# Kernel tuning notes

Hardware: AMD Instinct MI355X
Metric: run time of the kernel (lower is better)

Reference implementation:

```python
import jax, jax.numpy as jnp
import numpy as np

TEMP = 0.08
EPS = 1e-8
GAMMA = 0.99
BETA = 0.5 * (1.0 - GAMMA)  # alpha * (1 - gamma)
COS_EPS = 1e-8  # torch F.cosine_similarity norm-product clamp


def setup_inputs() -> dict:
    key = jax.random.key(0)
    k1, k2, k3 = jax.random.split(key, 3)
    B, D, C = 8192, 256, 7
    features = jax.random.normal(k1, (B, D), dtype=jnp.float32)
    labels = jax.random.randint(k2, (B,), 0, C)
    # orthogonal prototypes via QR, as in generate_orthogonal_vectors
    q, _ = jnp.linalg.qr(jax.random.normal(k3, (D, C), dtype=jnp.float32))
    prototypes = q.T  # [C, D]
    momentums = jnp.zeros((C, D), dtype=jnp.float32)
    return {"features": features, "labels": labels,
            "prototypes": prototypes, "momentums": momentums}


def _update_prototypes(features, labels, prototypes, momentums):
    # sequential EMA over the batch (repeated labels chain), as in the torch loop
    deltas = features - prototypes[labels]  # delta uses the OLD prototypes throughout

    def step(m, ld):
        l, d = ld
        return m.at[l].set(GAMMA * m[l] + BETA * d), None

    m_final, _ = jax.lax.scan(step, momentums, (labels, deltas))
    target = prototypes + m_final  # [C, D]
    q, _ = jnp.linalg.qr(target.T)  # reduced QR: [D, C]
    return q.T  # [C, D], re-orthogonalized prototypes


def reference(features, labels, prototypes, momentums):
    C = prototypes.shape[0]
    new_protos = _update_prototypes(features, labels, prototypes, momentums)

    feats = jnp.concatenate([features, new_protos], axis=0)          # [N, D]
    labs = jnp.concatenate([labels, jnp.arange(C, dtype=labels.dtype)])
    N = feats.shape[0]

    # cosine similarity matrix: dot / clamp(|x||y|, eps)  (matches F.cosine_similarity)
    nrm = jnp.linalg.norm(feats, axis=-1)                            # [N]
    sim = (feats @ feats.T) / jnp.maximum(nrm[:, None] * nrm[None, :], COS_EPS)
    scores = (1.0 + sim) * 0.5 + EPS

    offdiag = 1.0 - jnp.eye(N, dtype=scores.dtype)
    scores = scores * offdiag / TEMP
    scores = scores - jnp.max(scores)

    same = labs[:, None] == labs[None, :]                            # [N, N] bool
    pos_mask = same.astype(scores.dtype) * offdiag
    neg_mask = (~same).astype(scores.dtype)

    pos = jnp.sum(scores * pos_mask, axis=-1) / (jnp.sum(pos_mask, axis=-1) + EPS)
    neg = jnp.log(jnp.sum(jnp.exp(scores) * neg_mask, axis=-1) + EPS)
    loss = -pos + neg                                                # [N]

    m = loss > 0
    cnt = jnp.sum(m.astype(loss.dtype))
    mean_pos = jnp.sum(jnp.where(m, loss, 0.0)) / jnp.maximum(cnt, 1.0)
    return jnp.where(cnt > 0, mean_pos, jnp.array(0.0, loss.dtype))
```

## Files before the change

### kernel.cpp

```cpp
#include <hip/hip_runtime.h>
#include <stdint.h>

#define B    8192
#define D    256
#define C    7
#define NTOT 8199
#define NPAD 8320
#define NT   65
#define NBLK 2145
#define BETAC 0.005f
#define L2GAMMA (-0.0144995696951151f)

using f32x4  = __attribute__((ext_vector_type(4))) float;

__device__ __forceinline__ void async16(const void* src, void* dst) {
    __builtin_amdgcn_global_load_lds(
        (const __attribute__((address_space(1))) void*)src,
        (__attribute__((address_space(3))) void*)dst, 16, 0, 0);
}

__device__ __forceinline__ float score_of(float sim) {
    return fmaf(sim, 6.25f, 6.25f + 1.25e-7f);
}

#define WAITVM(N) asm volatile("s_waitcnt vmcnt(" #N ")" ::: "memory")
#define BARRIER() do { __builtin_amdgcn_s_barrier(); asm volatile("" ::: "memory"); } while(0)

__global__ void kprep(const int* __restrict__ labels, float* __restrict__ wbuf,
                      int* __restrict__ labs_ext, int* __restrict__ hist,
                      float* __restrict__ S, float* __restrict__ lossacc,
                      unsigned* __restrict__ ticket) {
    __shared__ int cnt[256 * 8];
    __shared__ int tot[8];
    int t = threadIdx.x;
    int lane = t & 63, w = t >> 6;
    for (int i = t; i < C * 256; i += 256) S[i] = 0.f;
    if (t == 0) { lossacc[0] = 0.f; lossacc[1] = 0.f; *ticket = 0u; }
    int lab[32];
    #pragma unroll
    for (int q = 0; q < 8; ++q) {
        int4 v = *(const int4*)(labels + t * 32 + q * 4);
        lab[q * 4 + 0] = v.x; lab[q * 4 + 1] = v.y;
        lab[q * 4 + 2] = v.z; lab[q * 4 + 3] = v.w;
    }
    int myc[8] = {0, 0, 0, 0, 0, 0, 0, 0};
    #pragma unroll
    for (int k = 0; k < 32; ++k) {
        #pragma unroll
        for (int cc = 0; cc < 7; ++cc) myc[cc] += (lab[k] == cc) ? 1 : 0;
    }
    #pragma unroll
    for (int cc = 0; cc < 8; ++cc) cnt[t * 8 + cc] = myc[cc];
    __syncthreads();
    for (int c = w; c < C; c += 4) {
        int v[4], partial = 0;
        #pragma unroll
        for (int k = 0; k < 4; ++k) { v[k] = cnt[(lane * 4 + k) * 8 + c]; partial += v[k]; }
        int inc = partial;
        #pragma unroll
        for (int d = 1; d < 64; d <<= 1) {
            int y = __shfl_up(inc, d);
            if (lane >= d) inc += y;
        }
        int run = inc - partial;
        #pragma unroll
        for (int k = 0; k < 4; ++k) { int tmp = v[k]; cnt[(lane * 4 + k) * 8 + c] = run; run += tmp; }
        if (lane == 63) { tot[c] = inc; hist[c] = inc; }
    }
    __syncthreads();
    #pragma unroll 4
    for (int k = 0; k < 32; ++k) {
        int idx = t * 32 + k;
        int c = lab[k];
        int r = ++cnt[t * 8 + c];
        int kk = tot[c] - r;
        wbuf[idx] = exp2f((float)kk * L2GAMMA);
    }
    for (int i = t; i < NPAD; i += 256)
        labs_ext[i] = (i < B) ? labels[i] : ((i < NTOT) ? (i - B) : -1);
}

__global__ void kaccnorm(const float* __restrict__ feats, const int* __restrict__ labels,
                         const float* __restrict__ wbuf, float* __restrict__ S,
                         unsigned* __restrict__ G32) {
    __shared__ float sacc[4][7][256];
    int tid = threadIdx.x, lane = tid & 63, wv = tid >> 6;
    float acc7[7][4] = {};
    int base = blockIdx.x * 32 + wv * 8;
    for (int k = 0; k < 8; ++k) {
        int row = base + k;
        const float4 v = *(const float4*)(feats + (size_t)row * 256 + lane * 4);
        float ss = v.x * v.x + v.y * v.y + v.z * v.z + v.w * v.w;
        #pragma unroll
        for (int off = 1; off < 64; off <<= 1) ss += __shfl_xor(ss, off);
        float rn = 1.f / sqrtf(ss);
        unsigned p = (unsigned)__builtin_amdgcn_cvt_pk_fp8_f32(v.x * rn, v.y * rn, 0, false);
        p = (unsigned)__builtin_amdgcn_cvt_pk_fp8_f32(v.z * rn, v.w * rn, (int)p, true);
        G32[(size_t)row * 64 + lane] = p;
        int c = labels[row];
        float wgt = wbuf[row];
        float w0 = v.x * wgt, w1 = v.y * wgt, w2 = v.z * wgt, w3 = v.w * wgt;
        #pragma unroll
        for (int cc = 0; cc < 7; ++cc)
            if (c == cc) { acc7[cc][0] += w0; acc7[cc][1] += w1; acc7[cc][2] += w2; acc7[cc][3] += w3; }
    }
    #pragma unroll
    for (int cc = 0; cc < 7; ++cc) {
        #pragma unroll
        for (int jj = 0; jj < 4; ++jj)
            sacc[wv][cc][lane * 4 + jj] = acc7[cc][jj];
    }
    __syncthreads();
    #pragma unroll
    for (int cc = 0; cc < 7; ++cc) {
        float s = sacc[0][cc][tid] + sacc[1][cc][tid] + sacc[2][cc][tid] + sacc[3][cc][tid];
        atomicAdd(&S[cc * 256 + tid], s);
    }
    if (blockIdx.x < NPAD - NTOT && tid < 64)
        G32[(size_t)(NTOT + blockIdx.x) * 64 + tid] = 0u;
}

__global__ void kproto(const float* __restrict__ S, const int* __restrict__ hist,
                       const float* __restrict__ protos, const float* __restrict__ moms,
                       unsigned char* __restrict__ G8) {
    __shared__ float A[256 * 8];
    __shared__ float V[256 * 8];
    __shared__ float vvs[8];
    __shared__ float bcast[8];
    int t = threadIdx.x;
    int lane = t & 63, w = t >> 6;
    #pragma unroll
    for (int c = 0; c < C; ++c) {
        float p = protos[c * 256 + t];
        float m0 = moms[c * 256 + t];
        float gn = exp2f((float)hist[c] * L2GAMMA);
        float mf = gn * m0 + BETAC * S[c * 256 + t] - 0.5f * (1.f - gn) * p;
        A[t * 8 + c] = p + mf;
        V[t * 8 + c] = 0.f;
    }
    __syncthreads();
    for (int j = 0; j < C; ++j) {
        if (w == 0) {
            float s = 0.f;
            for (int i = lane; i < 256; i += 64) {
                float a = (i >= j) ? A[i * 8 + j] : 0.f;
                s += a * a;
            }
            #pragma unroll
            for (int off = 32; off; off >>= 1) s += __shfl_xor(s, off);
            if (lane == 0) {
                float norm = sqrtf(s);
                float alpha = A[j * 8 + j];
                float beta = (alpha >= 0.f) ? -norm : norm;
                float vv = 2.f * beta * (beta - alpha);
                bcast[0] = alpha; bcast[1] = beta;
                bcast[2] = (vv > 0.f) ? 1.f : 0.f;
                vvs[j] = (vv > 0.f) ? vv : 1.f;
            }
        }
        __syncthreads();
        float alpha = bcast[0], valid = bcast[2];
        float beta = bcast[1];
        float vi = 0.f;
        if (valid != 0.f) {
            if (t == j) vi = alpha - beta;
            else if (t > j) vi = A[t * 8 + j];
        }
        V[t * 8 + j] = vi;
        __syncthreads();
        float vvj = vvs[j];
        for (int k = j + 1 + w; k < C; k += 4) {
            float cp = 0.f;
            for (int i = lane; i < 256; i += 64) cp += V[i * 8 + j] * A[i * 8 + k];
            #pragma unroll
            for (int off = 32; off; off >>= 1) cp += __shfl_xor(cp, off);
            float scale = 2.f * cp / vvj;
            for (int i = lane; i < 256; i += 64) A[i * 8 + k] -= scale * V[i * 8 + j];
        }
        __syncthreads();
    }
    #pragma unroll
    for (int c = 0; c < C; ++c) A[t * 8 + c] = (t == c) ? 1.f : 0.f;
    __syncthreads();
    for (int j = C - 1; j >= 0; --j) {
        float vvj = vvs[j];
        for (int k = w; k < C; k += 4) {
            float cp = 0.f;
            for (int i = lane; i < 256; i += 64) cp += V[i * 8 + j] * A[i * 8 + k];
            #pragma unroll
            for (int off = 32; off; off >>= 1) cp += __shfl_xor(cp, off);
            float scale = 2.f * cp / vvj;
            for (int i = lane; i < 256; i += 64) A[i * 8 + k] -= scale * V[i * 8 + j];
        }
        __syncthreads();
    }
    for (int c = w; c < C; c += 4) {
        float s = 0.f;
        for (int i = lane; i < 256; i += 64) { float a = A[i * 8 + c]; s += a * a; }
        #pragma unroll
        for (int off = 32; off; off >>= 1) s += __shfl_xor(s, off);
        if (lane == 0) bcast[c] = 1.f / sqrtf(s);
    }
    __syncthreads();
    #pragma unroll
    for (int c = 0; c < C; ++c) {
        int pk = __builtin_amdgcn_cvt_pk_fp8_f32(A[t * 8 + c] * bcast[c], 0.f, 0, false);
        G8[(size_t)(B + c) * 256 + t] = (unsigned char)(pk & 0xff);
    }
}

__global__ __launch_bounds__(512, 2) void kmain(const unsigned char* __restrict__ G,
                                                const int* __restrict__ labs,
                                                float* __restrict__ pP,
                                                float* __restrict__ pN) {
    __shared__ unsigned char Asm_[128 * 256];
    __shared__ unsigned char Bsm_[128 * 256];
    float* rowP = (float*)Asm_;
    float* rowN = rowP + 256;
    float* colP = rowN + 256;
    float* colN = colP + 512;

    int b0 = blockIdx.x;
    int xcd = b0 & 7, pos = b0 >> 3;
    int b = (xcd == 0) ? pos : (269 + (xcd - 1) * 268 + pos);

    int jt = (int)((sqrtf(8.f * (float)b + 1.f) - 1.f) * 0.5f);
    while ((jt * (jt + 1)) / 2 > b) --jt;
    while (((jt + 1) * (jt + 2)) / 2 <= b) ++jt;
    int it = b - (jt * (jt + 1)) / 2;

    int rowA = it * 128, rowB = jt * 128;
    int tid = threadIdx.x, lane = tid & 63, w8 = tid >> 6;
    int wr = w8 >> 1, wc = w8 & 1;
    int g4 = lane >> 4, q15 = lane & 15;

    const char* gb = (const char*)G;

    #pragma unroll
    for (int q = 0; q < 4; ++q) {
        int o = q * 8192 + tid * 16;
        int row = o >> 8, colb = o & 255;
        int sc = colb ^ ((row & 15) << 4);
        async16(gb + (size_t)(rowA + row) * 256 + sc, (char*)Asm_ + o);
    }
    #pragma unroll
    for (int q = 0; q < 4; ++q) {
        int o = q * 8192 + tid * 16;
        int row = o >> 8, colb = o & 255;
        int sc = colb ^ ((row & 15) << 4);
        async16(gb + (size_t)(rowB + row) * 256 + sc, (char*)Bsm_ + o);
    }

    int ljv[4];
    #pragma unroll
    for (int n = 0; n < 4; ++n) ljv[n] = labs[rowB + wc * 64 + n * 16 + q15];
    int4 lrow[2];
    #pragma unroll
    for (int m = 0; m < 2; ++m)
        lrow[m] = *(const int4*)(labs + rowA + wr * 32 + m * 16 + g4 * 4);

    f32x4 acc[2][4];
    #pragma unroll
    for (int m = 0; m < 2; ++m)
        #pragma unroll
        for (int n = 0; n < 4; ++n) acc[m][n] = 0.f;

    WAITVM(0);
    BARRIER();

    #pragma unroll
    for (int kk = 0; kk < 8; ++kk) {
        long af[2], bfr[4];
        int cb = (kk * 32 + g4 * 8) ^ (q15 << 4);
        #pragma unroll
        for (int m = 0; m < 2; ++m) {
            int r0 = wr * 32 + m * 16 + q15;
            af[m] = *(const long*)((const char*)Asm_ + r0 * 256 + cb);
        }
        #pragma unroll
        for (int n = 0; n < 4; ++n) {
            int r0 = wc * 64 + n * 16 + q15;
            bfr[n] = *(const long*)((const char*)Bsm_ + r0 * 256 + cb);
        }
        __builtin_amdgcn_s_setprio(1);
        #pragma unroll
        for (int m = 0; m < 2; ++m)
            #pragma unroll
            for (int n = 0; n < 4; ++n)
                acc[m][n] = __builtin_amdgcn_mfma_f32_16x16x32_fp8_fp8(af[m], bfr[n], acc[m][n], 0, 0, 0);
        __builtin_amdgcn_s_setprio(0);
    }

    __syncthreads();

    float cs[4] = {0.f, 0.f, 0.f, 0.f}, cn[4] = {0.f, 0.f, 0.f, 0.f};
    bool fastpath = (it != jt) && (jt != NT - 1);

#define EPI(VALIDEXPR)                                                         \
    _Pragma("unroll")                                                          \
    for (int m = 0; m < 2; ++m) {                                              \
        _Pragma("unroll")                                                      \
        for (int r = 0; r < 4; ++r) {                                          \
            int il = wr * 32 + m * 16 + g4 * 4 + r;                            \
            int i = rowA + il; (void)i;                                        \
            int li = ((const int*)&lrow[m])[r];                                \
            float ps = 0.f, ns = 0.f;                                          \
            _Pragma("unroll")                                                  \
            for (int n = 0; n < 4; ++n) {                                      \
                int j = rowB + wc * 64 + n * 16 + q15; (void)j;                \
                float sim = acc[m][n][r];                                      \
                float s = score_of(sim);                                       \
                float e = __expf(s);                                           \
                if (VALIDEXPR) {                                               \
                    if (li == ljv[n]) { ps += s; cs[n] += s; }                 \
                    else              { ns += e; cn[n] += e; }                 \
                }                                                              \
            }                                                                  \
            _Pragma("unroll")                                                  \
            for (int off = 1; off < 16; off <<= 1) {                           \
                ps += __shfl_xor(ps, off);                                     \
                ns += __shfl_xor(ns, off);                                     \
            }                                                                  \
            if (q15 == 0) { rowP[wc * 128 + il] = ps; rowN[wc * 128 + il] = ns; } \
        }                                                                      \
    }

    if (fastpath) { EPI(true); }
    else          { EPI(i < NTOT && j < NTOT && i != j); }
#undef EPI

    #pragma unroll
    for (int n = 0; n < 4; ++n) {
        float a = cs[n], bb = cn[n];
        a += __shfl_xor(a, 16); a += __shfl_xor(a, 32);
        bb += __shfl_xor(bb, 16); bb += __shfl_xor(bb, 32);
        if (g4 == 0) {
            colP[wr * 128 + wc * 64 + n * 16 + q15] = a;
            colN[wr * 128 + wc * 64 + n * 16 + q15] = bb;
        }
    }

    __syncthreads();
    if (tid < 128) {
        pP[(size_t)jt * NPAD + rowA + tid] = rowP[tid] + rowP[128 + tid];
        pN[(size_t)jt * NPAD + rowA + tid] = rowN[tid] + rowN[128 + tid];
    } else if (tid < 256 && it != jt) {
        int tt = tid - 128;
        pP[(size_t)it * NPAD + rowB + tt] = colP[tt] + colP[128 + tt] + colP[256 + tt] + colP[384 + tt];
        pN[(size_t)it * NPAD + rowB + tt] = colN[tt] + colN[128 + tt] + colN[256 + tt] + colN[384 + tt];
    }
}

__global__ void kreduce(const float* __restrict__ pP, const float* __restrict__ pN,
                        const int* __restrict__ hist, const int* __restrict__ labs,
                        float* __restrict__ lossacc, unsigned* __restrict__ ticket,
                        float* __restrict__ out) {
    int i = blockIdx.x * 256 + threadIdx.x;
    float lsum = 0.f, lcnt = 0.f;
    if (i < NTOT) {
        float sp = 0.f, sn = 0.f;
        #pragma unroll 5
        for (int c = 0; c < NT; ++c) {
            sp += pP[(size_t)c * NPAD + i];
            sn += pN[(size_t)c * NPAD + i];
        }
        float cnt = (float)hist[labs[i]];
        float pos = sp / (cnt + 1e-8f);
        float neg = logf(sn + 1e-8f);
        float loss = neg - pos;
        if (loss > 0.f) { lsum = loss; lcnt = 1.f; }
    }
    #pragma unroll
    for (int off = 1; off < 64; off <<= 1) {
        lsum += __shfl_xor(lsum, off);
        lcnt += __shfl_xor(lcnt, off);
    }
    __shared__ float s1[4], s2[4];
    int lane = threadIdx.x & 63, w = threadIdx.x >> 6;
    if (lane == 0) { s1[w] = lsum; s2[w] = lcnt; }
    __syncthreads();
    if (threadIdx.x == 0) {
        atomicAdd(&lossacc[0], s1[0] + s1[1] + s1[2] + s1[3]);
        atomicAdd(&lossacc[1], s2[0] + s2[1] + s2[2] + s2[3]);
        __threadfence();
        unsigned tk = atomicAdd(ticket, 1u);
        if (tk == 32) {
            float a = atomicAdd(&lossacc[0], 0.f);
            float c2 = atomicAdd(&lossacc[1], 0.f);
            out[0] = (c2 > 0.f) ? a / fmaxf(c2, 1.f) : 0.f;
        }
    }
}

extern "C" void kernel_launch(void* const* d_in, const int* in_sizes, int n_in,
                              void* d_out, int out_size, void* d_ws, size_t ws_size,
                              hipStream_t stream) {
    const float* feats  = (const float*)d_in[0];
    const int*   labels = (const int*)d_in[1];
    const float* protos = (const float*)d_in[2];
    const float* moms   = (const float*)d_in[3];
    float* out = (float*)d_out;

    char* ws = (char*)d_ws;
    float*    S_      = (float*)(ws + 0);
    int*      hist    = (int*)  (ws + 7168);
    float*    lossacc = (float*)(ws + 7200);
    unsigned* ticket  = (unsigned*)(ws + 7208);
    float*    wbuf    = (float*)(ws + 7296);
    int*      labs    = (int*)  (ws + 40064);
    unsigned char* G  = (unsigned char*)(ws + 73344);
    float*    pP      = (float*)(ws + 2203264);
    float*    pN      = (float*)(ws + 4366464);

    kprep<<<1, 256, 0, stream>>>(labels, wbuf, labs, hist, S_, lossacc, ticket);
    kaccnorm<<<256, 256, 0, stream>>>(feats, labels, wbuf, S_, (unsigned*)G);
    kproto<<<1, 256, 0, stream>>>(S_, hist, protos, moms, G);
    kmain<<<NBLK, 512, 0, stream>>>(G, labs, pP, pN);
    kreduce<<<33, 256, 0, stream>>>(pP, pN, hist, labs, lossacc, ticket, out);
}
```

Before: 105.0 us.

## Compute positive sums via per-class sums of normalized features instead of in GEMM

The positive term is computed algebraically: each row's sum of same-label similarities equals its dot product with the class sum of normalized features, so the main tile epilogue accumulates only masked exp for negatives. Per-class normalized-feature sums are built alongside the EMA accumulation, and the final reduce does a 256-wide dot per row. The single-block prep kernel is merged into the accumulation kernel, which now writes per-block partials instead of using atomics. The exp uses exp2 with folded constants. This risks precision differences, since the positive sum now comes from fp32 features rather than the fp8 similarities used in the GEMM.

```diff
diff --git a/kernel.cpp b/kernel.cpp
--- a/kernel.cpp
+++ b/kernel.cpp
@@ -10,6 +10,10 @@
 #define NBLK 2145
 #define BETAC 0.005f
 #define L2GAMMA (-0.0144995696951151f)
+#define KC   (6.25f + 1.25e-7f)
+#define EC1  9.016844005555771f
+#define EC0  9.016844185925551f
+#define KACCB 128
 
 using f32x4  = __attribute__((ext_vector_type(4))) float;
 
@@ -19,23 +23,21 @@
         (__attribute__((address_space(3))) void*)dst, 16, 0, 0);
 }
 
-__device__ __forceinline__ float score_of(float sim) {
-    return fmaf(sim, 6.25f, 6.25f + 1.25e-7f);
-}
-
 #define WAITVM(N) asm volatile("s_waitcnt vmcnt(" #N ")" ::: "memory")
 #define BARRIER() do { __builtin_amdgcn_s_barrier(); asm volatile("" ::: "memory"); } while(0)
 
-__global__ void kprep(const int* __restrict__ labels, float* __restrict__ wbuf,
-                      int* __restrict__ labs_ext, int* __restrict__ hist,
-                      float* __restrict__ S, float* __restrict__ lossacc,
-                      unsigned* __restrict__ ticket) {
+__global__ void kaccnorm(const float* __restrict__ feats, const int* __restrict__ labels,
+                         float* __restrict__ Spart, float* __restrict__ CSpart,
+                         unsigned* __restrict__ G32, int* __restrict__ labs_ext,
+                         int* __restrict__ hist, float* __restrict__ lossacc,
+                         unsigned* __restrict__ ticket) {
     __shared__ int cnt[256 * 8];
     __shared__ int tot[8];
-    int t = threadIdx.x;
-    int lane = t & 63, w = t >> 6;
-    for (int i = t; i < C * 256; i += 256) S[i] = 0.f;
-    if (t == 0) { lossacc[0] = 0.f; lossacc[1] = 0.f; *ticket = 0u; }
+    __shared__ float wrow[64];
+    __shared__ float sacc[4][7][256];
+    int t = threadIdx.x, lane = t & 63, w = t >> 6;
+    int bid = blockIdx.x;
+
     int lab[32];
     #pragma unroll
     for (int q = 0; q < 8; ++q) {
@@ -65,76 +67,98 @@
         int run = inc - partial;
         #pragma unroll
         for (int k = 0; k < 4; ++k) { int tmp = v[k]; cnt[(lane * 4 + k) * 8 + c] = run; run += tmp; }
-        if (lane == 63) { tot[c] = inc; hist[c] = inc; }
-    }
-    __syncthreads();
-    #pragma unroll 4
-    for (int k = 0; k < 32; ++k) {
-        int idx = t * 32 + k;
-        int c = lab[k];
-        int r = ++cnt[t * 8 + c];
-        int kk = tot[c] - r;
-        wbuf[idx] = exp2f((float)kk * L2GAMMA);
-    }
-    for (int i = t; i < NPAD; i += 256)
-        labs_ext[i] = (i < B) ? labels[i] : ((i < NTOT) ? (i - B) : -1);
-}
-
-__global__ void kaccnorm(const float* __restrict__ feats, const int* __restrict__ labels,
-                         const float* __restrict__ wbuf, float* __restrict__ S,
-                         unsigned* __restrict__ G32) {
-    __shared__ float sacc[4][7][256];
-    int tid = threadIdx.x, lane = tid & 63, wv = tid >> 6;
+        if (lane == 63) { tot[c] = inc; if (bid == 0) hist[c] = inc; }
+    }
+    __syncthreads();
+    if (t < 2) {
+        int ch = 2 * bid + t;
+        int loc[7];
+        #pragma unroll
+        for (int cc = 0; cc < 7; ++cc) loc[cc] = cnt[ch * 8 + cc];
+        for (int k = 0; k < 32; ++k) {
+            int c2 = labels[ch * 32 + k];
+            int r = ++loc[c2];
+            wrow[t * 32 + k] = exp2f((float)(tot[c2] - r) * L2GAMMA);
+        }
+    }
+    if (t < 64) labs_ext[bid * 64 + t] = labels[bid * 64 + t];
+    if (bid == 0) {
+        if (t == 0) { lossacc[0] = 0.f; lossacc[1] = 0.f; *ticket = 0u; }
+        if (t < 128) { int i2 = B + t; labs_ext[i2] = (i2 < NTOT) ? (i2 - B) : -1; }
+        for (int idx = t; idx < 121 * 64; idx += 256) G32[NTOT * 64 + idx] = 0u;
+    }
+    __syncthreads();
+
     float acc7[7][4] = {};
-    int base = blockIdx.x * 32 + wv * 8;
-    for (int k = 0; k < 8; ++k) {
+    float cs7[7][4] = {};
+    int base = bid * 64 + w * 16;
+    for (int k = 0; k < 16; ++k) {
         int row = base + k;
         const float4 v = *(const float4*)(feats + (size_t)row * 256 + lane * 4);
         float ss = v.x * v.x + v.y * v.y + v.z * v.z + v.w * v.w;
         #pragma unroll
         for (int off = 1; off < 64; off <<= 1) ss += __shfl_xor(ss, off);
         float rn = 1.f / sqrtf(ss);
-        unsigned p = (unsigned)__builtin_amdgcn_cvt_pk_fp8_f32(v.x * rn, v.y * rn, 0, false);
-        p = (unsigned)__builtin_amdgcn_cvt_pk_fp8_f32(v.z * rn, v.w * rn, (int)p, true);
+        float g0 = v.x * rn, g1 = v.y * rn, g2 = v.z * rn, g3 = v.w * rn;
+        unsigned p = (unsigned)__builtin_amdgcn_cvt_pk_fp8_f32(g0, g1, 0, false);
+        p = (unsigned)__builtin_amdgcn_cvt_pk_fp8_f32(g2, g3, (int)p, true);
         G32[(size_t)row * 64 + lane] = p;
         int c = labels[row];
-        float wgt = wbuf[row];
-        float w0 = v.x * wgt, w1 = v.y * wgt, w2 = v.z * wgt, w3 = v.w * wgt;
+        float wgt = wrow[w * 16 + k];
         #pragma unroll
         for (int cc = 0; cc < 7; ++cc)
-            if (c == cc) { acc7[cc][0] += w0; acc7[cc][1] += w1; acc7[cc][2] += w2; acc7[cc][3] += w3; }
-    }
-    #pragma unroll
-    for (int cc = 0; cc < 7; ++cc) {
-        #pragma unroll
-        for (int jj = 0; jj < 4; ++jj)
-            sacc[wv][cc][lane * 4 + jj] = acc7[cc][jj];
-    }
-    __syncthreads();
-    #pragma unroll
-    for (int cc = 0; cc < 7; ++cc) {
-        float s = sacc[0][cc][tid] + sacc[1][cc][tid] + sacc[2][cc][tid] + sacc[3][cc][tid];
-        atomicAdd(&S[cc * 256 + tid], s);
-    }
-    if (blockIdx.x < NPAD - NTOT && tid < 64)
-        G32[(size_t)(NTOT + blockIdx.x) * 64 + tid] = 0u;
-}
-
-__global__ void kproto(const float* __restrict__ S, const int* __restrict__ hist,
-                       const float* __restrict__ protos, const float* __restrict__ moms,
-                       unsigned char* __restrict__ G8) {
+            if (c == cc) {
+                acc7[cc][0] += wgt * v.x; acc7[cc][1] += wgt * v.y;
+                acc7[cc][2] += wgt * v.z; acc7[cc][3] += wgt * v.w;
+                cs7[cc][0] += g0; cs7[cc][1] += g1;
+                cs7[cc][2] += g2; cs7[cc][3] += g3;
+            }
+    }
+    #pragma unroll
+    for (int cc = 0; cc < 7; ++cc)
+        #pragma unroll
+        for (int jj = 0; jj < 4; ++jj) sacc[w][cc][lane * 4 + jj] = acc7[cc][jj];
+    __syncthreads();
+    #pragma unroll
+    for (int cc = 0; cc < 7; ++cc)
+        Spart[(size_t)bid * 1792 + cc * 256 + t] =
+            sacc[0][cc][t] + sacc[1][cc][t] + sacc[2][cc][t] + sacc[3][cc][t];
+    __syncthreads();
+    #pragma unroll
+    for (int cc = 0; cc < 7; ++cc)
+        #pragma unroll
+        for (int jj = 0; jj < 4; ++jj) sacc[w][cc][lane * 4 + jj] = cs7[cc][jj];
+    __syncthreads();
+    #pragma unroll
+    for (int cc = 0; cc < 7; ++cc)
+        CSpart[(size_t)bid * 1792 + cc * 256 + t] =
+            sacc[0][cc][t] + sacc[1][cc][t] + sacc[2][cc][t] + sacc[3][cc][t];
+}
+
+__global__ void kproto(const float* __restrict__ Spart, const float* __restrict__ CSpart,
+                       const int* __restrict__ hist, const float* __restrict__ protos,
+                       const float* __restrict__ moms, unsigned char* __restrict__ G8,
+                       float* __restrict__ CSfin, float* __restrict__ Pnorm) {
     __shared__ float A[256 * 8];
     __shared__ float V[256 * 8];
     __shared__ float vvs[8];
     __shared__ float bcast[8];
     int t = threadIdx.x;
     int lane = t & 63, w = t >> 6;
+    float ssum[7] = {}, cssum[7] = {};
+    for (int b2 = 0; b2 < KACCB; ++b2) {
+        #pragma unroll
+        for (int cc = 0; cc < 7; ++cc) {
+            ssum[cc]  += Spart[(size_t)b2 * 1792 + cc * 256 + t];
+            cssum[cc] += CSpart[(size_t)b2 * 1792 + cc * 256 + t];
+        }
+    }
     #pragma unroll
     for (int c = 0; c < C; ++c) {
         float p = protos[c * 256 + t];
         float m0 = moms[c * 256 + t];
         float gn = exp2f((float)hist[c] * L2GAMMA);
-        float mf = gn * m0 + BETAC * S[c * 256 + t] - 0.5f * (1.f - gn) * p;
+        float mf = gn * m0 + BETAC * ssum[c] - 0.5f * (1.f - gn) * p;
         A[t * 8 + c] = p + mf;
         V[t * 8 + c] = 0.f;
     }
@@ -204,21 +228,21 @@
     __syncthreads();
     #pragma unroll
     for (int c = 0; c < C; ++c) {
-        int pk = __builtin_amdgcn_cvt_pk_fp8_f32(A[t * 8 + c] * bcast[c], 0.f, 0, false);
+        float val = A[t * 8 + c] * bcast[c];
+        int pk = __builtin_amdgcn_cvt_pk_fp8_f32(val, 0.f, 0, false);
         G8[(size_t)(B + c) * 256 + t] = (unsigned char)(pk & 0xff);
+        Pnorm[c * 256 + t] = val;
+        CSfin[c * 256 + t] = cssum[c] + val;
     }
 }
 
 __global__ __launch_bounds__(512, 2) void kmain(const unsigned char* __restrict__ G,
                                                 const int* __restrict__ labs,
-                                                float* __restrict__ pP,
                                                 float* __restrict__ pN) {
     __shared__ unsigned char Asm_[128 * 256];
     __shared__ unsigned char Bsm_[128 * 256];
-    float* rowP = (float*)Asm_;
-    float* rowN = rowP + 256;
-    float* colP = rowN + 256;
-    float* colN = colP + 512;
+    float* rowN = (float*)Asm_;
+    float* colN = rowN + 256;
 
     int b0 = blockIdx.x;
     int xcd = b0 & 7, pos = b0 >> 3;
@@ -293,7 +317,7 @@
 
     __syncthreads();
 
-    float cs[4] = {0.f, 0.f, 0.f, 0.f}, cn[4] = {0.f, 0.f, 0.f, 0.f};
+    float cn[4] = {0.f, 0.f, 0.f, 0.f};
     bool fastpath = (it != jt) && (jt != NT - 1);
 
 #define EPI(VALIDEXPR)                                                         \
@@ -304,24 +328,19 @@
             int il = wr * 32 + m * 16 + g4 * 4 + r;                            \
             int i = rowA + il; (void)i;                                        \
             int li = ((const int*)&lrow[m])[r];                                \
-            float ps = 0.f, ns = 0.f;                                          \
+            float ns = 0.f;                                                    \
             _Pragma("unroll")                                                  \
             for (int n = 0; n < 4; ++n) {                                      \
                 int j = rowB + wc * 64 + n * 16 + q15; (void)j;                \
                 float sim = acc[m][n][r];                                      \
-                float s = score_of(sim);                                       \
-                float e = __expf(s);                                           \
-                if (VALIDEXPR) {                                               \
-                    if (li == ljv[n]) { ps += s; cs[n] += s; }                 \
-                    else              { ns += e; cn[n] += e; }                 \
-                }                                                              \
+                float e = exp2f(fmaf(sim, EC1, EC0));                          \
+                bool keep = (VALIDEXPR) && (li != ljv[n]);                     \
+                float me = keep ? e : 0.f;                                     \
+                ns += me; cn[n] += me;                                         \
             }                                                                  \
             _Pragma("unroll")                                                  \
-            for (int off = 1; off < 16; off <<= 1) {                           \
-                ps += __shfl_xor(ps, off);                                     \
-                ns += __shfl_xor(ns, off);                                     \
-            }                                                                  \
-            if (q15 == 0) { rowP[wc * 128 + il] = ps; rowN[wc * 128 + il] = ns; } \
+            for (int off = 1; off < 16; off <<= 1) ns += __shfl_xor(ns, off);  \
+            if (q15 == 0) rowN[wc * 128 + il] = ns;                            \
         }                                                                      \
     }
 
@@ -331,41 +350,61 @@
 
     #pragma unroll
     for (int n = 0; n < 4; ++n) {
-        float a = cs[n], bb = cn[n];
+        float a = cn[n];
         a += __shfl_xor(a, 16); a += __shfl_xor(a, 32);
-        bb += __shfl_xor(bb, 16); bb += __shfl_xor(bb, 32);
-        if (g4 == 0) {
-            colP[wr * 128 + wc * 64 + n * 16 + q15] = a;
-            colN[wr * 128 + wc * 64 + n * 16 + q15] = bb;
-        }
+        if (g4 == 0) colN[wr * 128 + wc * 64 + n * 16 + q15] = a;
     }
 
     __syncthreads();
     if (tid < 128) {
-        pP[(size_t)jt * NPAD + rowA + tid] = rowP[tid] + rowP[128 + tid];
         pN[(size_t)jt * NPAD + rowA + tid] = rowN[tid] + rowN[128 + tid];
     } else if (tid < 256 && it != jt) {
         int tt = tid - 128;
-        pP[(size_t)it * NPAD + rowB + tt] = colP[tt] + colP[128 + tt] + colP[256 + tt] + colP[384 + tt];
         pN[(size_t)it * NPAD + rowB + tt] = colN[tt] + colN[128 + tt] + colN[256 + tt] + colN[384 + tt];
     }
 }
 
-__global__ void kreduce(const float* __restrict__ pP, const float* __restrict__ pN,
+__global__ void kreduce(const float* __restrict__ pN, const float* __restrict__ feats,
+                        const float* __restrict__ Pnorm, const float* __restrict__ CSfin,
                         const int* __restrict__ hist, const int* __restrict__ labs,
                         float* __restrict__ lossacc, unsigned* __restrict__ ticket,
                         float* __restrict__ out) {
-    int i = blockIdx.x * 256 + threadIdx.x;
+    __shared__ float cls[7 * 264];
+    int tid = threadIdx.x;
+    for (int idx = tid; idx < 7 * 256; idx += 256)
+        cls[(idx >> 8) * 264 + (idx & 255)] = CSfin[idx];
+    __syncthreads();
+
+    int i = blockIdx.x * 256 + tid;
     float lsum = 0.f, lcnt = 0.f;
     if (i < NTOT) {
-        float sp = 0.f, sn = 0.f;
+        float sn = 0.f;
         #pragma unroll 5
-        for (int c = 0; c < NT; ++c) {
-            sp += pP[(size_t)c * NPAD + i];
-            sn += pN[(size_t)c * NPAD + i];
-        }
-        float cnt = (float)hist[labs[i]];
-        float pos = sp / (cnt + 1e-8f);
+        for (int c = 0; c < NT; ++c) sn += pN[(size_t)c * NPAD + i];
+
+        int c = labs[i];
+        const float* cv = cls + c * 264;
+        float dot = 0.f;
+        if (i < B) {
+            float ss = 0.f;
+            const float* fr = feats + (size_t)i * 256;
+            for (int k4 = 0; k4 < 64; ++k4) {
+                float4 v = *(const float4*)(fr + k4 * 4);
+                float4 cvv = *(const float4*)(cv + k4 * 4);
+                ss += v.x * v.x + v.y * v.y + v.z * v.z + v.w * v.w;
+                dot += v.x * cvv.x + v.y * cvv.y + v.z * cvv.z + v.w * cvv.w;
+            }
+            dot *= 1.f / sqrtf(ss);
+        } else {
+            const float* pr = Pnorm + (size_t)(i - B) * 256;
+            for (int k4 = 0; k4 < 64; ++k4) {
+                float4 v = *(const float4*)(pr + k4 * 4);
+                float4 cvv = *(const float4*)(cv + k4 * 4);
+                dot += v.x * cvv.x + v.y * cvv.y + v.z * cvv.z + v.w * cvv.w;
+            }
+        }
+        float cnt = (float)hist[c];
+        float pos = (6.25f * (dot - 1.f) + cnt * KC) / (cnt + 1e-8f);
         float neg = logf(sn + 1e-8f);
         float loss = neg - pos;
         if (loss > 0.f) { lsum = loss; lcnt = 1.f; }
@@ -376,10 +415,10 @@
         lcnt += __shfl_xor(lcnt, off);
     }
     __shared__ float s1[4], s2[4];
-    int lane = threadIdx.x & 63, w = threadIdx.x >> 6;
+    int lane = tid & 63, w = tid >> 6;
     if (lane == 0) { s1[w] = lsum; s2[w] = lcnt; }
     __syncthreads();
-    if (threadIdx.x == 0) {
+    if (tid == 0) {
         atomicAdd(&lossacc[0], s1[0] + s1[1] + s1[2] + s1[3]);
         atomicAdd(&lossacc[1], s2[0] + s2[1] + s2[2] + s2[3]);
         __threadfence();
@@ -402,19 +441,21 @@
     float* out = (float*)d_out;
 
     char* ws = (char*)d_ws;
-    float*    S_      = (float*)(ws + 0);
-    int*      hist    = (int*)  (ws + 7168);
-    float*    lossacc = (float*)(ws + 7200);
-    unsigned* ticket  = (unsigned*)(ws + 7208);
-    float*    wbuf    = (float*)(ws + 7296);
-    int*      labs    = (int*)  (ws + 40064);
-    unsigned char* G  = (unsigned char*)(ws + 73344);
-    float*    pP      = (float*)(ws + 2203264);
-    float*    pN      = (float*)(ws + 4366464);
-
-    kprep<<<1, 256, 0, stream>>>(labels, wbuf, labs, hist, S_, lossacc, ticket);
-    kaccnorm<<<256, 256, 0, stream>>>(feats, labels, wbuf, S_, (unsigned*)G);
-    kproto<<<1, 256, 0, stream>>>(S_, hist, protos, moms, G);
-    kmain<<<NBLK, 512, 0, stream>>>(G, labs, pP, pN);
-    kreduce<<<33, 256, 0, stream>>>(pP, pN, hist, labs, lossacc, ticket, out);
-}
+    int*      hist    = (int*)  (ws + 0);
+    float*    lossacc = (float*)(ws + 32);
+    unsigned* ticket  = (unsigned*)(ws + 40);
+    float*    CSfin   = (float*)(ws + 64);
+    float*    Pnorm   = (float*)(ws + 7232);
+    int*      labs    = (int*)  (ws + 14400);
+    float*    Spart   = (float*)(ws + 47744);
+    float*    CSpart  = (float*)(ws + 965248);
+    unsigned char* G  = (unsigned char*)(ws + 1882752);
+    float*    pN      = (float*)(ws + 4012672);
+
+    kaccnorm<<<KACCB, 256, 0, stream>>>(feats, labels, Spart, CSpart,
+                                        (unsigned*)G, labs, hist, lossacc, ticket);
+    kproto<<<1, 256, 0, stream>>>(Spart, CSpart, hist, protos, moms, G, CSfin, Pnorm);
+    kmain<<<NBLK, 512, 0, stream>>>(G, labs, pN);
+    kreduce<<<33, 256, 0, stream>>>(pN, feats, Pnorm, CSfin, hist, labs,
+                                    lossacc, ticket, out);
+}
```

Result: slower. 147.0 us (+40.0%).

## Fold prototype QR into main kernel with flag-gated proto tiles

Applied to the files above, without the earlier changes.

Removes the separate single-block kproto launch. Block 0 of kmain now does the prototype update and Householder QR, then publishes a flag. Tiles that need the prototype rows spin on that flag and reload those rows via atomics into shared memory. This hides the serial QR step behind the bulk similarity tiles and saves a launch. Smaller changes: exp(s) is replaced by a single exp2 of a folded affine term, the padding zeroing moves into kprep, and zero atomics are skipped. The risks are a spin-wait that deadlocks if block 0 is never scheduled, and added work on block 0.

```diff
diff --git a/kernel.cpp b/kernel.cpp
--- a/kernel.cpp
+++ b/kernel.cpp
@@ -10,6 +10,9 @@
 #define NBLK 2145
 #define BETAC 0.005f
 #define L2GAMMA (-0.0144995696951151f)
+#define KC   (6.25f + 1.25e-7f)
+#define EC1  9.016844005555771f
+#define EC0  9.016844185925551f
 
 using f32x4  = __attribute__((ext_vector_type(4))) float;
 
@@ -19,23 +22,17 @@
         (__attribute__((address_space(3))) void*)dst, 16, 0, 0);
 }
 
-__device__ __forceinline__ float score_of(float sim) {
-    return fmaf(sim, 6.25f, 6.25f + 1.25e-7f);
-}
-
 #define WAITVM(N) asm volatile("s_waitcnt vmcnt(" #N ")" ::: "memory")
 #define BARRIER() do { __builtin_amdgcn_s_barrier(); asm volatile("" ::: "memory"); } while(0)
 
 __global__ void kprep(const int* __restrict__ labels, float* __restrict__ wbuf,
                       int* __restrict__ labs_ext, int* __restrict__ hist,
-                      float* __restrict__ S, float* __restrict__ lossacc,
-                      unsigned* __restrict__ ticket) {
+                      float* __restrict__ zbase, unsigned* __restrict__ G32) {
     __shared__ int cnt[256 * 8];
     __shared__ int tot[8];
     int t = threadIdx.x;
     int lane = t & 63, w = t >> 6;
-    for (int i = t; i < C * 256; i += 256) S[i] = 0.f;
-    if (t == 0) { lossacc[0] = 0.f; lossacc[1] = 0.f; *ticket = 0u; }
+    for (int i = t; i < 1804; i += 256) zbase[i] = 0.f;
     int lab[32];
     #pragma unroll
     for (int q = 0; q < 8; ++q) {
@@ -73,11 +70,11 @@
         int idx = t * 32 + k;
         int c = lab[k];
         int r = ++cnt[t * 8 + c];
-        int kk = tot[c] - r;
-        wbuf[idx] = exp2f((float)kk * L2GAMMA);
+        wbuf[idx] = exp2f((float)(tot[c] - r) * L2GAMMA);
     }
     for (int i = t; i < NPAD; i += 256)
         labs_ext[i] = (i < B) ? labels[i] : ((i < NTOT) ? (i - B) : -1);
+    for (int i = t; i < 121 * 64; i += 256) G32[NTOT * 64 + i] = 0u;
 }
 
 __global__ void kaccnorm(const float* __restrict__ feats, const int* __restrict__ labels,
@@ -99,122 +96,39 @@
         G32[(size_t)row * 64 + lane] = p;
         int c = labels[row];
         float wgt = wbuf[row];
-        float w0 = v.x * wgt, w1 = v.y * wgt, w2 = v.z * wgt, w3 = v.w * wgt;
         #pragma unroll
         for (int cc = 0; cc < 7; ++cc)
-            if (c == cc) { acc7[cc][0] += w0; acc7[cc][1] += w1; acc7[cc][2] += w2; acc7[cc][3] += w3; }
-    }
-    #pragma unroll
-    for (int cc = 0; cc < 7; ++cc) {
-        #pragma unroll
-        for (int jj = 0; jj < 4; ++jj)
-            sacc[wv][cc][lane * 4 + jj] = acc7[cc][jj];
-    }
+            if (c == cc) {
+                acc7[cc][0] += wgt * v.x; acc7[cc][1] += wgt * v.y;
+                acc7[cc][2] += wgt * v.z; acc7[cc][3] += wgt * v.w;
+            }
+    }
+    #pragma unroll
+    for (int cc = 0; cc < 7; ++cc)
+        #pragma unroll
+        for (int jj = 0; jj < 4; ++jj) sacc[wv][cc][lane * 4 + jj] = acc7[cc][jj];
     __syncthreads();
     #pragma unroll
     for (int cc = 0; cc < 7; ++cc) {
         float s = sacc[0][cc][tid] + sacc[1][cc][tid] + sacc[2][cc][tid] + sacc[3][cc][tid];
-        atomicAdd(&S[cc * 256 + tid], s);
-    }
-    if (blockIdx.x < NPAD - NTOT && tid < 64)
-        G32[(size_t)(NTOT + blockIdx.x) * 64 + tid] = 0u;
-}
-
-__global__ void kproto(const float* __restrict__ S, const int* __restrict__ hist,
-                       const float* __restrict__ protos, const float* __restrict__ moms,
-                       unsigned char* __restrict__ G8) {
-    __shared__ float A[256 * 8];
-    __shared__ float V[256 * 8];
+        if (s != 0.f) atomicAdd(&S[cc * 256 + tid], s);
+    }
+}
+
+__global__ __launch_bounds__(512, 2) void kmain(const unsigned char* __restrict__ G,
+                                                unsigned* __restrict__ G32w,
+                                                const int* __restrict__ labs,
+                                                float* __restrict__ pP,
+                                                float* __restrict__ pN,
+                                                const float* __restrict__ S,
+                                                const int* __restrict__ hist,
+                                                const float* __restrict__ protos,
+                                                const float* __restrict__ moms,
+                                                unsigned* __restrict__ flag) {
+    __shared__ unsigned char Asm_[128 * 256];
+    __shared__ unsigned char Bsm_[128 * 256];
     __shared__ float vvs[8];
     __shared__ float bcast[8];
-    int t = threadIdx.x;
-    int lane = t & 63, w = t >> 6;
-    #pragma unroll
-    for (int c = 0; c < C; ++c) {
-        float p = protos[c * 256 + t];
-        float m0 = moms[c * 256 + t];
-        float gn = exp2f((float)hist[c] * L2GAMMA);
-        float mf = gn * m0 + BETAC * S[c * 256 + t] - 0.5f * (1.f - gn) * p;
-        A[t * 8 + c] = p + mf;
-        V[t * 8 + c] = 0.f;
-    }
-    __syncthreads();
-    for (int j = 0; j < C; ++j) {
-        if (w == 0) {
-            float s = 0.f;
-            for (int i = lane; i < 256; i += 64) {
-                float a = (i >= j) ? A[i * 8 + j] : 0.f;
-                s += a * a;
-            }
-            #pragma unroll
-            for (int off = 32; off; off >>= 1) s += __shfl_xor(s, off);
-            if (lane == 0) {
-                float norm = sqrtf(s);
-                float alpha = A[j * 8 + j];
-                float beta = (alpha >= 0.f) ? -norm : norm;
-                float vv = 2.f * beta * (beta - alpha);
-                bcast[0] = alpha; bcast[1] = beta;
-                bcast[2] = (vv > 0.f) ? 1.f : 0.f;
-                vvs[j] = (vv > 0.f) ? vv : 1.f;
-            }
-        }
-        __syncthreads();
-        float alpha = bcast[0], valid = bcast[2];
-        float beta = bcast[1];
-        float vi = 0.f;
-        if (valid != 0.f) {
-            if (t == j) vi = alpha - beta;
-            else if (t > j) vi = A[t * 8 + j];
-        }
-        V[t * 8 + j] = vi;
-        __syncthreads();
-        float vvj = vvs[j];
-        for (int k = j + 1 + w; k < C; k += 4) {
-            float cp = 0.f;
-            for (int i = lane; i < 256; i += 64) cp += V[i * 8 + j] * A[i * 8 + k];
-            #pragma unroll
-            for (int off = 32; off; off >>= 1) cp += __shfl_xor(cp, off);
-            float scale = 2.f * cp / vvj;
-            for (int i = lane; i < 256; i += 64) A[i * 8 + k] -= scale * V[i * 8 + j];
-        }
-        __syncthreads();
-    }
-    #pragma unroll
-    for (int c = 0; c < C; ++c) A[t * 8 + c] = (t == c) ? 1.f : 0.f;
-    __syncthreads();
-    for (int j = C - 1; j >= 0; --j) {
-        float vvj = vvs[j];
-        for (int k = w; k < C; k += 4) {
-            float cp = 0.f;
-            for (int i = lane; i < 256; i += 64) cp += V[i * 8 + j] * A[i * 8 + k];
-            #pragma unroll
-            for (int off = 32; off; off >>= 1) cp += __shfl_xor(cp, off);
-            float scale = 2.f * cp / vvj;
-            for (int i = lane; i < 256; i += 64) A[i * 8 + k] -= scale * V[i * 8 + j];
-        }
-        __syncthreads();
-    }
-    for (int c = w; c < C; c += 4) {
-        float s = 0.f;
-        for (int i = lane; i < 256; i += 64) { float a = A[i * 8 + c]; s += a * a; }
-        #pragma unroll
-        for (int off = 32; off; off >>= 1) s += __shfl_xor(s, off);
-        if (lane == 0) bcast[c] = 1.f / sqrtf(s);
-    }
-    __syncthreads();
-    #pragma unroll
-    for (int c = 0; c < C; ++c) {
-        int pk = __builtin_amdgcn_cvt_pk_fp8_f32(A[t * 8 + c] * bcast[c], 0.f, 0, false);
-        G8[(size_t)(B + c) * 256 + t] = (unsigned char)(pk & 0xff);
-    }
-}
-
-__global__ __launch_bounds__(512, 2) void kmain(const unsigned char* __restrict__ G,
-                                                const int* __restrict__ labs,
-                                                float* __restrict__ pP,
-                                                float* __restrict__ pN) {
-    __shared__ unsigned char Asm_[128 * 256];
-    __shared__ unsigned char Bsm_[128 * 256];
     float* rowP = (float*)Asm_;
     float* rowN = rowP + 256;
     float* colP = rowN + 256;
@@ -233,8 +147,117 @@
     int tid = threadIdx.x, lane = tid & 63, w8 = tid >> 6;
     int wr = w8 >> 1, wc = w8 & 1;
     int g4 = lane >> 4, q15 = lane & 15;
-
     const char* gb = (const char*)G;
+
+    if (b == 0) {
+        float* Aq = (float*)Asm_;
+        float* Vq = (float*)Bsm_;
+        int t = tid, w = tid >> 6, ln = tid & 63;
+        if (tid < 256) {
+            #pragma unroll
+            for (int c = 0; c < C; ++c) {
+                float p = protos[c * 256 + t];
+                float m0 = moms[c * 256 + t];
+                float gn = exp2f((float)hist[c] * L2GAMMA);
+                float mf = gn * m0 + BETAC * S[c * 256 + t] - 0.5f * (1.f - gn) * p;
+                Aq[t * 8 + c] = p + mf;
+                Vq[t * 8 + c] = 0.f;
+            }
+        }
+        __syncthreads();
+        for (int j = 0; j < C; ++j) {
+            if (tid < 64) {
+                float s = 0.f;
+                for (int i = tid; i < 256; i += 64) {
+                    float a = (i >= j) ? Aq[i * 8 + j] : 0.f;
+                    s += a * a;
+                }
+                #pragma unroll
+                for (int off = 32; off; off >>= 1) s += __shfl_xor(s, off);
+                if (tid == 0) {
+                    float norm = sqrtf(s);
+                    float alpha = Aq[j * 8 + j];
+                    float beta = (alpha >= 0.f) ? -norm : norm;
+                    float vv = 2.f * beta * (beta - alpha);
+                    bcast[0] = alpha; bcast[1] = beta;
+                    bcast[2] = (vv > 0.f) ? 1.f : 0.f;
+                    vvs[j] = (vv > 0.f) ? vv : 1.f;
+                }
+            }
+            __syncthreads();
+            if (tid < 256) {
+                float alpha = bcast[0], valid = bcast[2];
+                float beta = bcast[1];
+                float vi = 0.f;
+                if (valid != 0.f) {
+                    if (t == j) vi = alpha - beta;
+                    else if (t > j) vi = Aq[t * 8 + j];
+                }
+                Vq[t * 8 + j] = vi;
+            }
+            __syncthreads();
+            if (tid < 256) {
+                float vvj = vvs[j];
+                for (int k = j + 1 + w; k < C; k += 4) {
+                    float cp = 0.f;
+                    for (int i = ln; i < 256; i += 64) cp += Vq[i * 8 + j] * Aq[i * 8 + k];
+                    #pragma unroll
+                    for (int off = 32; off; off >>= 1) cp += __shfl_xor(cp, off);
+                    float scale = 2.f * cp / vvj;
+                    for (int i = ln; i < 256; i += 64) Aq[i * 8 + k] -= scale * Vq[i * 8 + j];
+                }
+            }
+            __syncthreads();
+        }
+        if (tid < 256) {
+            #pragma unroll
+            for (int c = 0; c < C; ++c) Aq[t * 8 + c] = (t == c) ? 1.f : 0.f;
+        }
+        __syncthreads();
+        for (int j = C - 1; j >= 0; --j) {
+            if (tid < 256) {
+                float vvj = vvs[j];
+                for (int k = w; k < C; k += 4) {
+                    float cp = 0.f;
+                    for (int i = ln; i < 256; i += 64) cp += Vq[i * 8 + j] * Aq[i * 8 + k];
+                    #pragma unroll
+                    for (int off = 32; off; off >>= 1) cp += __shfl_xor(cp, off);
+                    float scale = 2.f * cp / vvj;
+                    for (int i = ln; i < 256; i += 64) Aq[i * 8 + k] -= scale * Vq[i * 8 + j];
+                }
+            }
+            __syncthreads();
+        }
+        if (tid < 256) {
+            for (int c = w; c < C; c += 4) {
+                float s = 0.f;
+                for (int i = ln; i < 256; i += 64) { float a = Aq[i * 8 + c]; s += a * a; }
+                #pragma unroll
+                for (int off = 32; off; off >>= 1) s += __shfl_xor(s, off);
+                if (ln == 0) bcast[c] = 1.f / sqrtf(s);
+            }
+        }
+        __syncthreads();
+        if (tid < 256) {
+            unsigned char* G8 = (unsigned char*)G32w;
+            #pragma unroll
+            for (int c = 0; c < C; ++c) {
+                float val = Aq[t * 8 + c] * bcast[c];
+                int pk = __builtin_amdgcn_cvt_pk_fp8_f32(val, 0.f, 0, false);
+                G8[(size_t)(B + c) * 256 + t] = (unsigned char)(pk & 0xff);
+            }
+        }
+        __syncthreads();
+        if (tid == 0) { __threadfence(); atomicExch(flag, 1u); }
+    }
+
+    bool protoTile = (jt == NT - 1);
+    if (protoTile) {
+        if (tid == 0) {
+            while (atomicAdd(flag, 0u) == 0u) __builtin_amdgcn_s_sleep(32);
+        }
+        __syncthreads();
+    }
 
     #pragma unroll
     for (int q = 0; q < 4; ++q) {
@@ -267,6 +290,17 @@
 
     WAITVM(0);
     BARRIER();
+
+    if (protoTile) {
+        if (tid < 448) {
+            int c = tid >> 6, l = tid & 63;
+            unsigned v = atomicAdd(&G32w[(size_t)(B + c) * 64 + l], 0u);
+            int off = c * 256 + ((((l >> 2) ^ c) << 4) | ((l & 3) << 2));
+            *(unsigned*)((char*)Bsm_ + off) = v;
+            if (it == NT - 1) *(unsigned*)((char*)Asm_ + off) = v;
+        }
+        __syncthreads();
+    }
 
     #pragma unroll
     for (int kk = 0; kk < 8; ++kk) {
@@ -309,8 +343,8 @@
             for (int n = 0; n < 4; ++n) {                                      \
                 int j = rowB + wc * 64 + n * 16 + q15; (void)j;                \
                 float sim = acc[m][n][r];                                      \
-                float s = score_of(sim);                                       \
-                float e = __expf(s);                                           \
+                float s = fmaf(sim, 6.25f, KC);                                \
+                float e = exp2f(fmaf(sim, EC1, EC0));                          \
                 if (VALIDEXPR) {                                               \
                     if (li == ljv[n]) { ps += s; cs[n] += s; }                 \
                     else              { ns += e; cn[n] += e; }                 \
@@ -406,15 +440,16 @@
     int*      hist    = (int*)  (ws + 7168);
     float*    lossacc = (float*)(ws + 7200);
     unsigned* ticket  = (unsigned*)(ws + 7208);
-    float*    wbuf    = (float*)(ws + 7296);
-    int*      labs    = (int*)  (ws + 40064);
-    unsigned char* G  = (unsigned char*)(ws + 73344);
-    float*    pP      = (float*)(ws + 2203264);
-    float*    pN      = (float*)(ws + 4366464);
-
-    kprep<<<1, 256, 0, stream>>>(labels, wbuf, labs, hist, S_, lossacc, ticket);
+    unsigned* flag    = (unsigned*)(ws + 7212);
+    int*      labs    = (int*)  (ws + 7296);
+    float*    wbuf    = (float*)(ws + 40576);
+    unsigned char* G  = (unsigned char*)(ws + 73472);
+    float*    pP      = (float*)(ws + 2203392);
+    float*    pN      = (float*)(ws + 4366592);
+
+    kprep<<<1, 256, 0, stream>>>(labels, wbuf, labs, hist, (float*)ws, (unsigned*)G);
     kaccnorm<<<256, 256, 0, stream>>>(feats, labels, wbuf, S_, (unsigned*)G);
-    kproto<<<1, 256, 0, stream>>>(S_, hist, protos, moms, G);
-    kmain<<<NBLK, 512, 0, stream>>>(G, labs, pP, pN);
+    kmain<<<NBLK, 512, 0, stream>>>(G, (unsigned*)G, labs, pP, pN, S_, hist,
+                                    protos, moms, flag);
     kreduce<<<33, 256, 0, stream>>>(pP, pN, hist, labs, lossacc, ticket, out);
 }
```

After: 90.59 us. 1.16x faster.
